# Kernel optimization log

Measured on AMD Instinct MI355X. Metric: run time of the kernel, lower is better.

## Reference

```python
import jax, jax.numpy as jnp
import numpy as np

TEMPERATURE = 0.07
EPS = 1e-8  # torch CosineSimilarity eps


def setup_inputs() -> dict:
    key = jax.random.key(0)
    features = jax.random.normal(key, (16, 1024, 512), dtype=jnp.float32)
    return {"features": features}


def reference(features):
    """Vectorized equivalent of the original double Python loop.

    For each b and each t in [1, T-2]:
      anchor = f[b,t], positive = f[b,t+1]
      negatives = all frames j with j < t-1 or j >= t+2  (excludes t-1, t, t+1)
      loss_bt = -log( exp(cos(a,p)/T) / (exp(cos(a,p)/T) + sum_j exp(cos(a,n_j)/T)) )
    Returns mean over all (b, t) pairs (neg pool is non-empty for all t when T > 3).
    """
    B, T, D = features.shape
    norm = jnp.maximum(jnp.linalg.norm(features, axis=-1, keepdims=True), EPS)
    n = features / norm  # [B, T, D]
    # full pairwise cosine-sim logits, scaled by temperature
    sim = jnp.einsum('btd,bsd->bts', n, n) / TEMPERATURE  # [B, T, T]

    t_idx = jnp.arange(1, T - 1)            # anchors t = 1 .. T-2
    j_idx = jnp.arange(T)
    # negatives: j in [0, t-1) union [t+2, T)  -> excludes t-1, t, t+1
    neg_mask = (j_idx[None, :] < t_idx[:, None] - 1) | (j_idx[None, :] >= t_idx[:, None] + 2)  # [T-2, T]

    logits = sim[:, 1:T - 1, :]                                   # [B, T-2, T]
    pos = logits[:, jnp.arange(T - 2), jnp.arange(2, T)]          # sim[b, t, t+1] -> [B, T-2]
    neg_logits = jnp.where(neg_mask[None], logits, -jnp.inf)
    lse_neg = jax.nn.logsumexp(neg_logits, axis=-1)               # log sum_j exp(neg_sim)
    # -log(exp(pos)/(exp(pos)+negsum)) = logaddexp(pos, lse_neg) - pos
    loss_bt = jnp.logaddexp(pos, lse_neg) - pos                   # [B, T-2]
    return jnp.mean(loss_bt)
```

## Files before the change

kernel.cpp:

```cpp
#include <hip/hip_runtime.h>
#include <hip/hip_bf16.h>

#define B_ 16
#define T_ 1024
#define D_ 512
#define EPS_ 1e-8f
#define SCALE2 20.609929155566063f
#define LN2_ 0.6931471805599453f

#define BM 128
#define BN 128
#define NKIT 16

typedef __attribute__((ext_vector_type(8))) short short8;
typedef __attribute__((ext_vector_type(4))) float floatx4;

typedef __attribute__((address_space(1))) const unsigned int g_u32;
typedef __attribute__((address_space(3))) unsigned int l_u32;

__device__ __forceinline__ void glds16(const void* g, void* l) {
    __builtin_amdgcn_global_load_lds((g_u32*)g, (l_u32*)l, 16, 0, 0);
}

__device__ __forceinline__ unsigned short f2bf(float x) {
    unsigned u = __float_as_uint(x);
    return (unsigned short)((u + 0x7fffu + ((u >> 16) & 1u)) >> 16);
}

__global__ __launch_bounds__(256) void norm_kernel(const float* __restrict__ f,
                                                   unsigned short* __restrict__ nrm,
                                                   float* __restrict__ rs_g,
                                                   float* __restrict__ rp_g,
                                                   float* __restrict__ out) {
    const int gi = blockIdx.x * 256 + threadIdx.x;
    if (gi < B_ * T_) { rs_g[gi] = 0.0f; rp_g[gi] = 0.0f; }
    if (gi == 0) out[0] = 0.0f;

    const int row  = blockIdx.x * 4 + (threadIdx.x >> 6);
    const int lane = threadIdx.x & 63;
    const size_t off = (size_t)row * D_ + lane * 8;
    const float4 v0 = *(const float4*)(f + off);
    const float4 v1 = *(const float4*)(f + off + 4);
    float ss = v0.x*v0.x + v0.y*v0.y + v0.z*v0.z + v0.w*v0.w
             + v1.x*v1.x + v1.y*v1.y + v1.z*v1.z + v1.w*v1.w;
    #pragma unroll
    for (int o = 32; o >= 1; o >>= 1) ss += __shfl_xor(ss, o, 64);
    const float sc = 1.0f / fmaxf(sqrtf(ss), EPS_);
    ushort4 w0, w1;
    w0.x = f2bf(v0.x*sc); w0.y = f2bf(v0.y*sc); w0.z = f2bf(v0.z*sc); w0.w = f2bf(v0.w*sc);
    w1.x = f2bf(v1.x*sc); w1.y = f2bf(v1.y*sc); w1.z = f2bf(v1.z*sc); w1.w = f2bf(v1.w*sc);
    *(ushort4*)(nrm + off)     = w0;
    *(ushort4*)(nrm + off + 4) = w1;
}

__global__ __launch_bounds__(256, 4) void loss_kernel(const unsigned short* __restrict__ nrm,
                                                      float* __restrict__ rs_g,
                                                      float* __restrict__ rp_g) {
    const int b  = blockIdx.y;
    const int t0 = blockIdx.x * BM;
    const int j0 = blockIdx.z * BN;
    const char* base = (const char*)(nrm + (size_t)b * T_ * D_);

    __shared__ __align__(16) unsigned short Al[2][BM * 32];
    __shared__ __align__(16) unsigned short Bl[2][BN * 32];

    const int tid = threadIdx.x;
    const int w   = tid >> 6;
    const int l   = tid & 63;

    const int r  = l >> 2;
    const int cc = l & 3;
    const int g  = cc ^ ((r >> 1) & 3);
    const char* sA0 = base + (size_t)(t0 + w * 32 +      r) * 1024 + g * 16;
    const char* sA1 = base + (size_t)(t0 + w * 32 + 16 + r) * 1024 + g * 16;
    const char* sB0 = base + (size_t)(j0 + w * 32 +      r) * 1024 + g * 16;
    const char* sB1 = base + (size_t)(j0 + w * 32 + 16 + r) * 1024 + g * 16;

#define ISSUE(P) do {                                             \
    glds16(sA0, (char*)Al[P] + w * 2048);                         \
    glds16(sA1, (char*)Al[P] + w * 2048 + 1024);                  \
    glds16(sB0, (char*)Bl[P] + w * 2048);                         \
    glds16(sB1, (char*)Bl[P] + w * 2048 + 1024);                  \
    sA0 += 64; sA1 += 64; sB0 += 64; sB1 += 64;                   \
} while (0)

    const int wr = w >> 1, wc = w & 1;
    const int m  = l & 15;
    const int kq = l >> 4;
    const int rdsw = (kq ^ ((m >> 1) & 3)) << 4;
    const int raoff = (wr * 64 + m) * 64 + rdsw;
    const int rboff = (wc * 64 + m) * 64 + rdsw;

    floatx4 acc[4][4] = {};

    ISSUE(0);

    #pragma unroll 2
    for (int kit = 0; kit < NKIT; ++kit) {
        __syncthreads();
        if (kit + 1 < NKIT) ISSUE((kit + 1) & 1);

        const char* pa = (const char*)Al[kit & 1] + raoff;
        const char* pb = (const char*)Bl[kit & 1] + rboff;
        short8 af[4], bf[4];
        #pragma unroll
        for (int mi = 0; mi < 4; ++mi) af[mi] = *(const short8*)(pa + mi * 1024);
        #pragma unroll
        for (int ni = 0; ni < 4; ++ni) bf[ni] = *(const short8*)(pb + ni * 1024);

        #pragma unroll
        for (int mi = 0; mi < 4; ++mi)
            #pragma unroll
            for (int ni = 0; ni < 4; ++ni)
                acc[mi][ni] = __builtin_amdgcn_mfma_f32_16x16x32_bf16(
                    af[mi], bf[ni], acc[mi][ni], 0, 0, 0);
    }
#undef ISSUE

    const int lrow = l >> 4;
    const int lcol = l & 15;
    const int bT   = b * T_;

    #pragma unroll
    for (int mi = 0; mi < 4; ++mi) {
        #pragma unroll
        for (int rg = 0; rg < 4; ++rg) {
            const int t = t0 + wr * 64 + mi * 16 + lrow * 4 + rg;
            float rsum = 0.f, rp = 0.f;
            #pragma unroll
            for (int ni = 0; ni < 4; ++ni) {
                const int j  = j0 + wc * 64 + ni * 16 + lcol;
                const float s2 = acc[mi][ni][rg] * SCALE2;
                const float e  = exp2f(s2);
                if (j < t - 1 || j > t + 1) rsum += e;
                if (j == t + 1)             rp   = s2;
            }
            #pragma unroll
            for (int o = 8; o >= 1; o >>= 1) {
                rsum += __shfl_xor(rsum, o, 64);
                rp   += __shfl_xor(rp,   o, 64);
            }
            if (lcol == 0) {
                atomicAdd(&rs_g[bT + t], rsum);
                if (rp != 0.0f) atomicAdd(&rp_g[bT + t], rp);
            }
        }
    }
}

__global__ __launch_bounds__(256) void fin_kernel(const float* __restrict__ rs_g,
                                                  const float* __restrict__ rp_g,
                                                  float* __restrict__ out) {
    const int idx = blockIdx.x * 256 + threadIdx.x;
    float v = 0.0f;
    if (idx < B_ * T_) {
        const int t = idx & (T_ - 1);
        if (t >= 1 && t <= T_ - 2) {
            const float p2 = rp_g[idx];
            const float s  = rs_g[idx];
            v = (log2f(exp2f(p2) + s) - p2) * LN2_;
        }
    }
    #pragma unroll
    for (int o = 32; o >= 1; o >>= 1) v += __shfl_xor(v, o, 64);
    __shared__ float ws_[4];
    if ((threadIdx.x & 63) == 0) ws_[threadIdx.x >> 6] = v;
    __syncthreads();
    if (threadIdx.x == 0) {
        const float scale = 1.0f / (float)(B_ * (T_ - 2));
        atomicAdd(out, (ws_[0] + ws_[1] + ws_[2] + ws_[3]) * scale);
    }
}

extern "C" void kernel_launch(void* const* d_in, const int* in_sizes, int n_in,
                              void* d_out, int out_size, void* d_ws, size_t ws_size,
                              hipStream_t stream) {
    const float* feat = (const float*)d_in[0];
    float* out = (float*)d_out;

    unsigned short* nrm = (unsigned short*)d_ws;
    float* rs_g = (float*)((char*)d_ws + (size_t)B_ * T_ * D_ * sizeof(unsigned short));
    float* rp_g = rs_g + B_ * T_;

    norm_kernel<<<B_ * T_ / 4, 256, 0, stream>>>(feat, nrm, rs_g, rp_g, out);
    loss_kernel<<<dim3(T_ / BM, B_, T_ / BN), 256, 0, stream>>>(nrm, rs_g, rp_g);
    fin_kernel<<<(B_ * T_ + 255) / 256, 256, 0, stream>>>(rs_g, rp_g, out);
}
```

Baseline: 107.2 us.

## Switch normalized features to FP8 e4m3 and use scaled MFMA 16x16x128

Normalized features are stored as FP8 e4m3, pre-scaled by 16 to use more of the e4m3 range, instead of bf16. The loss GEMM now uses the MX-scaled f8f6f4 MFMA with K=128 and a 2^-4 scale per operand (SCL 0x7B) to undo the pre-scaling. LDS tiles, the swizzle and the load addressing are reworked for 128-byte K chunks, and occupancy hints drop to 2 blocks. This halves operand bytes and raises MFMA throughput. The cost is much lower precision in cosine similarities that are then amplified by 1/0.07 inside exp, so the loss may drift from the reference.

```diff
diff --git a/kernel.cpp b/kernel.cpp
--- a/kernel.cpp
+++ b/kernel.cpp
@@ -1,5 +1,6 @@
 #include <hip/hip_runtime.h>
 #include <hip/hip_bf16.h>
+#include <hip/hip_fp8.h>
 
 #define B_ 16
 #define T_ 1024
@@ -10,9 +11,11 @@
 
 #define BM 128
 #define BN 128
-#define NKIT 16
-
-typedef __attribute__((ext_vector_type(8))) short short8;
+#define NKIT 4
+#define SCL 0x7B7B7B7B
+
+typedef __attribute__((ext_vector_type(4))) int   int4v;
+typedef __attribute__((ext_vector_type(8))) int   int8v;
 typedef __attribute__((ext_vector_type(4))) float floatx4;
 
 typedef __attribute__((address_space(1))) const unsigned int g_u32;
@@ -22,13 +25,13 @@
     __builtin_amdgcn_global_load_lds((g_u32*)g, (l_u32*)l, 16, 0, 0);
 }
 
-__device__ __forceinline__ unsigned short f2bf(float x) {
-    unsigned u = __float_as_uint(x);
-    return (unsigned short)((u + 0x7fffu + ((u >> 16) & 1u)) >> 16);
+__device__ __forceinline__ unsigned char f2e4m3(float x) {
+    __hip_fp8_e4m3 q(x);
+    return (unsigned char)q.__x;
 }
 
 __global__ __launch_bounds__(256) void norm_kernel(const float* __restrict__ f,
-                                                   unsigned short* __restrict__ nrm,
+                                                   unsigned char* __restrict__ nrm,
                                                    float* __restrict__ rs_g,
                                                    float* __restrict__ rp_g,
                                                    float* __restrict__ out) {
@@ -45,15 +48,20 @@
              + v1.x*v1.x + v1.y*v1.y + v1.z*v1.z + v1.w*v1.w;
     #pragma unroll
     for (int o = 32; o >= 1; o >>= 1) ss += __shfl_xor(ss, o, 64);
-    const float sc = 1.0f / fmaxf(sqrtf(ss), EPS_);
-    ushort4 w0, w1;
-    w0.x = f2bf(v0.x*sc); w0.y = f2bf(v0.y*sc); w0.z = f2bf(v0.z*sc); w0.w = f2bf(v0.w*sc);
-    w1.x = f2bf(v1.x*sc); w1.y = f2bf(v1.y*sc); w1.z = f2bf(v1.z*sc); w1.w = f2bf(v1.w*sc);
-    *(ushort4*)(nrm + off)     = w0;
-    *(ushort4*)(nrm + off + 4) = w1;
-}
-
-__global__ __launch_bounds__(256, 4) void loss_kernel(const unsigned short* __restrict__ nrm,
+    const float sc = 16.0f / fmaxf(sqrtf(ss), EPS_);
+    unsigned int w0 =  (unsigned int)f2e4m3(v0.x*sc)
+                    | ((unsigned int)f2e4m3(v0.y*sc) << 8)
+                    | ((unsigned int)f2e4m3(v0.z*sc) << 16)
+                    | ((unsigned int)f2e4m3(v0.w*sc) << 24);
+    unsigned int w1 =  (unsigned int)f2e4m3(v1.x*sc)
+                    | ((unsigned int)f2e4m3(v1.y*sc) << 8)
+                    | ((unsigned int)f2e4m3(v1.z*sc) << 16)
+                    | ((unsigned int)f2e4m3(v1.w*sc) << 24);
+    uint2 w; w.x = w0; w.y = w1;
+    *(uint2*)(nrm + (size_t)row * D_ + lane * 8) = w;
+}
+
+__global__ __launch_bounds__(256, 2) void loss_kernel(const unsigned char* __restrict__ nrm,
                                                       float* __restrict__ rs_g,
                                                       float* __restrict__ rp_g) {
     const int b  = blockIdx.y;
@@ -61,59 +69,71 @@
     const int j0 = blockIdx.z * BN;
     const char* base = (const char*)(nrm + (size_t)b * T_ * D_);
 
-    __shared__ __align__(16) unsigned short Al[2][BM * 32];
-    __shared__ __align__(16) unsigned short Bl[2][BN * 32];
+    __shared__ __align__(16) char Al[2][16384];
+    __shared__ __align__(16) char Bl[2][16384];
 
     const int tid = threadIdx.x;
     const int w   = tid >> 6;
     const int l   = tid & 63;
 
-    const int r  = l >> 2;
-    const int cc = l & 3;
-    const int g  = cc ^ ((r >> 1) & 3);
-    const char* sA0 = base + (size_t)(t0 + w * 32 +      r) * 1024 + g * 16;
-    const char* sA1 = base + (size_t)(t0 + w * 32 + 16 + r) * 1024 + g * 16;
-    const char* sB0 = base + (size_t)(j0 + w * 32 +      r) * 1024 + g * 16;
-    const char* sB1 = base + (size_t)(j0 + w * 32 + 16 + r) * 1024 + g * 16;
-
-#define ISSUE(P) do {                                             \
-    glds16(sA0, (char*)Al[P] + w * 2048);                         \
-    glds16(sA1, (char*)Al[P] + w * 2048 + 1024);                  \
-    glds16(sB0, (char*)Bl[P] + w * 2048);                         \
-    glds16(sB1, (char*)Bl[P] + w * 2048 + 1024);                  \
-    sA0 += 64; sA1 += 64; sB0 += 64; sB1 += 64;                   \
+    const int r8l = l >> 3;
+    const int gch = (l & 7) ^ ((l >> 4) & 3);
+    const char* sA[4];
+    const char* sB[4];
+    #pragma unroll
+    for (int i = 0; i < 4; ++i) {
+        sA[i] = base + (size_t)(t0 + w * 32 + i * 8 + r8l) * 512 + gch * 16;
+        sB[i] = base + (size_t)(j0 + w * 32 + i * 8 + r8l) * 512 + gch * 16;
+    }
+
+#define ISSUE(P, KIT) do {                                                \
+    _Pragma("unroll")                                                     \
+    for (int i_ = 0; i_ < 4; ++i_) {                                      \
+        glds16(sA[i_] + (KIT) * 128, (char*)Al[P] + w * 4096 + i_ * 1024);\
+        glds16(sB[i_] + (KIT) * 128, (char*)Bl[P] + w * 4096 + i_ * 1024);\
+    }                                                                     \
 } while (0)
 
     const int wr = w >> 1, wc = w & 1;
     const int m  = l & 15;
     const int kq = l >> 4;
-    const int rdsw = (kq ^ ((m >> 1) & 3)) << 4;
-    const int raoff = (wr * 64 + m) * 64 + rdsw;
-    const int rboff = (wc * 64 + m) * 64 + rdsw;
+    const int p0 = (2 * kq) ^ ((m >> 1) & 3);
+    const int rd0 = m * 128 + p0 * 16;
+    const int rd1 = m * 128 + (p0 ^ 1) * 16;
 
     floatx4 acc[4][4] = {};
 
-    ISSUE(0);
-
-    #pragma unroll 2
+    ISSUE(0, 0);
+
+    #pragma unroll
     for (int kit = 0; kit < NKIT; ++kit) {
         __syncthreads();
-        if (kit + 1 < NKIT) ISSUE((kit + 1) & 1);
-
-        const char* pa = (const char*)Al[kit & 1] + raoff;
-        const char* pb = (const char*)Bl[kit & 1] + rboff;
-        short8 af[4], bf[4];
-        #pragma unroll
-        for (int mi = 0; mi < 4; ++mi) af[mi] = *(const short8*)(pa + mi * 1024);
-        #pragma unroll
-        for (int ni = 0; ni < 4; ++ni) bf[ni] = *(const short8*)(pb + ni * 1024);
+        if (kit + 1 < NKIT) ISSUE((kit + 1) & 1, kit + 1);
+
+        const char* As = (const char*)Al[kit & 1] + wr * 8192;
+        const char* Bs = (const char*)Bl[kit & 1] + wc * 8192;
+        int8v af[4], bf[4];
+        #pragma unroll
+        for (int mi = 0; mi < 4; ++mi) {
+            int4v lo = *(const int4v*)(As + mi * 2048 + rd0);
+            int4v hi = *(const int4v*)(As + mi * 2048 + rd1);
+            af[mi] = __builtin_shufflevector(lo, hi, 0, 1, 2, 3, 4, 5, 6, 7);
+        }
+        #pragma unroll
+        for (int ni = 0; ni < 4; ++ni) {
+            int4v lo = *(const int4v*)(Bs + ni * 2048 + rd0);
+            int4v hi = *(const int4v*)(Bs + ni * 2048 + rd1);
+            bf[ni] = __builtin_shufflevector(lo, hi, 0, 1, 2, 3, 4, 5, 6, 7);
+        }
 
         #pragma unroll
         for (int mi = 0; mi < 4; ++mi)
             #pragma unroll
             for (int ni = 0; ni < 4; ++ni)
-                acc[mi][ni] = __builtin_amdgcn_mfma_f32_16x16x32_bf16(
-                    af[mi], bf[ni], acc[mi][ni], 0, 0, 0);
+                acc[mi][ni] = __builtin_amdgcn_mfma_scale_f32_16x16x128_f8f6f4(
+                    af[mi], bf[ni], acc[mi][ni],
+                    0, 0,
+                    0, SCL, 0, SCL);
     }
 #undef ISSUE
 
@@ -178,8 +198,8 @@
     const float* feat = (const float*)d_in[0];
     float* out = (float*)d_out;
 
-    unsigned short* nrm = (unsigned short*)d_ws;
-    float* rs_g = (float*)((char*)d_ws + (size_t)B_ * T_ * D_ * sizeof(unsigned short));
+    unsigned char* nrm = (unsigned char*)d_ws;
+    float* rs_g = (float*)((char*)d_ws + (size_t)B_ * T_ * D_);
     float* rp_g = rs_g + B_ * T_;
 
     norm_kernel<<<B_ * T_ / 4, 256, 0, stream>>>(feat, nrm, rs_g, rp_g, out);
```

Result: no change. 105.3 us (-1.8%).
